# Performance work log

Measured on AMD Instinct MI355X. Metric: run time of the kernel, lower is better.

Reference implementation:

```python
import jax, jax.numpy as jnp
import numpy as np

H = 32        # query heads
KVH = 8       # key/value heads
D = 64        # head_dim
HID = 2048
B, S = 2, 2048

def rotate_half(x):
    x1, x2 = x[..., :D // 2], x[..., D // 2:]
    return jnp.concatenate((-x2, x1), axis=-1)

def setup_inputs() -> dict:
    key = jax.random.key(0)
    ks = jax.random.split(key, 7)
    scale = 1.0 / np.sqrt(HID)
    return {
        "x": jax.random.normal(ks[0], (B, S, HID), jnp.float32),
        "cos": jax.random.uniform(ks[1], (S, D), jnp.float32),
        "sin": jax.random.uniform(ks[2], (S, D), jnp.float32),
        "wq": jax.random.normal(ks[3], (HID, H * D), jnp.float32) * scale,
        "wk": jax.random.normal(ks[4], (HID, KVH * D), jnp.float32) * scale,
        "wv": jax.random.normal(ks[5], (HID, KVH * D), jnp.float32) * scale,
        "wo": jax.random.normal(ks[6], (HID, HID), jnp.float32) * scale,
    }

def reference(x, cos, sin, wq, wk, wv, wo):
    b, s, _ = x.shape
    # QKV projections -> [b, heads, s, d]
    q = (x @ wq).reshape(b, s, H, D).transpose(0, 2, 1, 3)
    k = (x @ wk).reshape(b, s, KVH, D).transpose(0, 2, 1, 3)
    v = (x @ wv).reshape(b, s, KVH, D).transpose(0, 2, 1, 3)
    # RoPE (cos/sin broadcast over batch and heads)
    c = cos[None, None, :, :]
    si = sin[None, None, :, :]
    q = q * c + rotate_half(q) * si
    k = k * c + rotate_half(k) * si
    # GQA: expand kv heads (repeat_interleave on head axis)
    g = H // KVH
    k = jnp.repeat(k, g, axis=1)
    v = jnp.repeat(v, g, axis=1)
    # causal SDPA
    scores = jnp.einsum("bhqd,bhkd->bhqk", q, k) / np.sqrt(D).astype(np.float32)
    causal = jnp.tril(jnp.ones((s, s), dtype=bool))
    scores = jnp.where(causal[None, None], scores, jnp.finfo(scores.dtype).min)
    attn = jax.nn.softmax(scores, axis=-1)
    out = jnp.einsum("bhqk,bhkd->bhqd", attn, v)
    out = out.transpose(0, 2, 1, 3).reshape(b, s, H * D)
    return out @ wo
```

## Files before the change

### kernel.cpp

```cpp
#include <hip/hip_runtime.h>
#include <stdint.h>

#define B_ 2
#define S_ 2048
#define H_ 32
#define KVH_ 8
#define D_ 64
#define HID_ 2048

typedef float f32x4 __attribute__((ext_vector_type(4)));
typedef float f32x16 __attribute__((ext_vector_type(16)));
typedef short bf16x8 __attribute__((ext_vector_type(8)));
typedef unsigned short u16;
typedef unsigned short u16x4 __attribute__((ext_vector_type(4)));
typedef unsigned short u16x8 __attribute__((ext_vector_type(8)));
typedef unsigned int u32;
typedef unsigned int u32x2 __attribute__((ext_vector_type(2)));
typedef unsigned int u32x4 __attribute__((ext_vector_type(4)));

__device__ __forceinline__ u16 f2b(float f) {
  unsigned u = __builtin_bit_cast(unsigned, f);
  u += 0x7fffu + ((u >> 16) & 1u);
  return (u16)(u >> 16);
}
__device__ __forceinline__ float b2f(u16 h) {
  unsigned u = ((unsigned)h) << 16;
  return __builtin_bit_cast(float, u);
}
__device__ __forceinline__ void gl_lds16(const void* g, void* l) {
  __builtin_amdgcn_global_load_lds(
      (const __attribute__((address_space(1))) unsigned*)g,
      (__attribute__((address_space(3))) unsigned*)l, 16, 0, 0);
}
__device__ __forceinline__ f32x4 mfma16(bf16x8 a, bf16x8 b, f32x4 c) {
  return __builtin_amdgcn_mfma_f32_16x16x32_bf16(a, b, c, 0, 0, 0);
}
__device__ __forceinline__ f32x16 mfma32(bf16x8 a, bf16x8 b, f32x16 c) {
  return __builtin_amdgcn_mfma_f32_32x32x16_bf16(a, b, c, 0, 0, 0);
}
__device__ __forceinline__ u32 cvtpk(float lo, float hi) {
  u32 r;
  asm("v_cvt_pk_bf16_f32 %0, %1, %2" : "=v"(r) : "v"(lo), "v"(hi));
  return r;
}
__device__ __forceinline__ float fast_exp2(float x) {
#if __has_builtin(__builtin_amdgcn_exp2f)
  return __builtin_amdgcn_exp2f(x);
#else
  return exp2f(x);
#endif
}
__device__ __forceinline__ void swap32(u32 a, u32 b, u32& x, u32& y) {
#if __has_builtin(__builtin_amdgcn_permlane32_swap)
  auto r = __builtin_amdgcn_permlane32_swap(a, b, false, false);
  x = r[0];
  y = r[1];
#else
  u32 sa = (u32)__shfl_xor((int)a, 32), sb = (u32)__shfl_xor((int)b, 32);
  bool hib = (threadIdx.x & 32) != 0;
  x = hib ? sb : a;
  y = hib ? b : sa;
#endif
}

__global__ __launch_bounds__(256) void k_cvt(const float* __restrict__ src,
                                             u16* __restrict__ dst, int n4) {
  int i = blockIdx.x * 256 + threadIdx.x;
  if (i >= n4) return;
  f32x4 v = *(const f32x4*)(src + (size_t)i * 4);
  u16x4 o;
  o[0] = f2b(v[0]); o[1] = f2b(v[1]); o[2] = f2b(v[2]); o[3] = f2b(v[3]);
  *(u16x4*)(dst + (size_t)i * 4) = o;
}

__global__ __launch_bounds__(256) void k_transpose(const float* __restrict__ src,
                                                   u16* __restrict__ dst,
                                                   int K, int N) {
  __shared__ float t[32][33];
  int n0 = blockIdx.x * 32, k0 = blockIdx.y * 32;
  int tt = threadIdx.x;
  int r = tt >> 3, c4 = (tt & 7) << 2;
  f32x4 v = *(const f32x4*)(src + (size_t)(k0 + r) * N + n0 + c4);
  t[r][c4 + 0] = v[0]; t[r][c4 + 1] = v[1];
  t[r][c4 + 2] = v[2]; t[r][c4 + 3] = v[3];
  __syncthreads();
  u16x4 o;
  o[0] = f2b(t[c4 + 0][r]); o[1] = f2b(t[c4 + 1][r]);
  o[2] = f2b(t[c4 + 2][r]); o[3] = f2b(t[c4 + 3][r]);
  *(u16x4*)(dst + (size_t)(n0 + r) * K + k0 + c4) = o;
}

__device__ __forceinline__ void stage64(const u16* __restrict__ G, int rowbase,
                                        int K, int kt, u16* unit, int tid) {
  int r = tid >> 3, sl = tid & 7;
  gl_lds16(G + (size_t)(rowbase + r) * K + kt * 64 + ((sl ^ (r & 7)) << 3),
           (char*)unit + tid * 16);
}

template <int BN, int OUTF32>
__global__ __launch_bounds__(512, 1) void k_gemm8(const u16* __restrict__ A,
                                                  const u16* __restrict__ BT,
                                                  float* __restrict__ Cf,
                                                  u16* __restrict__ Cb,
                                                  int M, int N, int K) {
  constexpr int ATILE = 256 * 64;
  constexpr int BTILE = BN * 64;
  constexpr int BU = BN / 64;
  constexpr int WN = (BN == 128) ? 2 : 4;
  constexpr int NI = (BN == 192) ? 3 : 4;
  constexpr int MI = (BN == 128) ? 4 : 8;
  constexpr int MIP = MI / 4;
  __shared__ __align__(16) u16 sm[2 * ATILE + 2 * BTILE];
  const int tid = threadIdx.x;
  const int l = tid & 63;
  const int lg = (l >> 4) & 3, lr = l & 15;
  const int w = tid >> 6;
  const int wm = w / WN, wn = w % WN;

  const int nwg = gridDim.x;
  const int cpx = nwg >> 3;
  const int bid = blockIdx.x;
  const int swz = (bid & 7) * cpx + (bid >> 3);
  const int ntn = N / BN;
  const int bm = swz / ntn, bn = swz % ntn;
  const int m0 = bm << 8, n0 = bn * BN;

  const u16* Ag = A + (size_t)m0 * K;
  const u16* Bg = BT + (size_t)n0 * K;
  u16* As = sm;
  u16* Bs = sm + 2 * ATILE;

  const int nt = K >> 6;
  f32x4 acc[MI][NI] = {};

#pragma unroll
  for (int u = 0; u < 4; ++u) stage64(Ag, u * 64, K, 0, As + u * 4096, tid);
#pragma unroll
  for (int u = 0; u < BU; ++u) stage64(Bg, u * 64, K, 0, Bs + u * 4096, tid);
  stage64(Ag, 0, K, 1, As + ATILE, tid);
  stage64(Ag, 64, K, 1, As + ATILE + 4096, tid);
  asm volatile("s_waitcnt vmcnt(2)" ::: "memory");
  __builtin_amdgcn_s_barrier();
  asm volatile("" ::: "memory");

  for (int t = 0; t < nt; ++t) {
    const int cur = t & 1;
    u16* Ac = As + cur * ATILE;
    u16* Bc = Bs + cur * BTILE;
    u16* An = As + (cur ^ 1) * ATILE;
    u16* Bn = Bs + (cur ^ 1) * BTILE;
    bf16x8 bc[NI][2];
#pragma unroll
    for (int q = 0; q < 4; ++q) {
      bf16x8 af[MIP][2];
#pragma unroll
      for (int mi2 = 0; mi2 < MIP; ++mi2)
#pragma unroll
        for (int ks = 0; ks < 2; ++ks) {
          int row = wm * (MI * 16) + (q * MIP + mi2) * 16 + lr;
          int slot = (ks * 4 + lg) ^ (lr & 7);
          af[mi2][ks] = *(const bf16x8*)&Ac[row * 64 + slot * 8];
        }
      if (q == 0) {
#pragma unroll
        for (int ni = 0; ni < NI; ++ni)
#pragma unroll
          for (int ks = 0; ks < 2; ++ks) {
            int row = wn * (NI * 16) + ni * 16 + lr;
            int slot = (ks * 4 + lg) ^ (lr & 7);
            bc[ni][ks] = *(const bf16x8*)&Bc[row * 64 + slot * 8];
          }
      }
      if (t + 1 < nt) {
        if (q == 0) {
          stage64(Ag, 128, K, t + 1, An + 2 * 4096, tid);
          stage64(Ag, 192, K, t + 1, An + 3 * 4096, tid);
        } else if (q == 1) {
          stage64(Bg, 0, K, t + 1, Bn, tid);
          stage64(Bg, 64, K, t + 1, Bn + 4096, tid);
        } else if (q == 2) {
          if (BU >= 3) stage64(Bg, 128, K, t + 1, Bn + 2 * 4096, tid);
          if (BU >= 4) stage64(Bg, 192, K, t + 1, Bn + 3 * 4096, tid);
        }
      }
      __builtin_amdgcn_s_barrier();
      asm volatile("" ::: "memory");
      __builtin_amdgcn_s_setprio(1);
#pragma unroll
      for (int mi2 = 0; mi2 < MIP; ++mi2)
#pragma unroll
        for (int ni = 0; ni < NI; ++ni)
#pragma unroll
          for (int ks = 0; ks < 2; ++ks)
            acc[q * MIP + mi2][ni] =
                mfma16(af[mi2][ks], bc[ni][ks], acc[q * MIP + mi2][ni]);
      __builtin_amdgcn_s_setprio(0);
      if (q == 3) {
        if (t + 2 < nt) {
          stage64(Ag, 0, K, t + 2, Ac, tid);
          stage64(Ag, 64, K, t + 2, Ac + 4096, tid);
          asm volatile("s_waitcnt vmcnt(2)" ::: "memory");
        } else if (t + 1 < nt) {
          asm volatile("s_waitcnt vmcnt(0)" ::: "memory");
        }
      }
      __builtin_amdgcn_s_barrier();
      asm volatile("" ::: "memory");
    }
  }

#pragma unroll
  for (int mi = 0; mi < MI; ++mi)
#pragma unroll
    for (int ni = 0; ni < NI; ++ni)
#pragma unroll
      for (int j = 0; j < 4; ++j) {
        size_t row = (size_t)m0 + wm * (MI * 16) + mi * 16 + lg * 4 + j;
        size_t col = (size_t)n0 + wn * (NI * 16) + ni * 16 + lr;
        if (OUTF32)
          Cf[row * N + col] = acc[mi][ni][j];
        else
          Cb[row * N + col] = f2b(acc[mi][ni][j]);
      }
}

__global__ __launch_bounds__(256) void k_rope(const u16* __restrict__ qkv,
                                              const float* __restrict__ cosb,
                                              const float* __restrict__ sinb,
                                              u16* __restrict__ Qr,
                                              u16* __restrict__ Kr) {
  int task = blockIdx.x * 4 + (threadIdx.x >> 6);
  int l = threadIdx.x & 63;
  int head = task % (H_ + KVH_);
  int row = task / (H_ + KVH_);
  int b = row >> 11, s = row & (S_ - 1);
  float c = cosb[s * 64 + l], si = sinb[s * 64 + l];
  const u16* base = qkv + (size_t)row * 3072;
  float val;
  if (head < H_)
    val = b2f(base[head * 64 + l]);
  else
    val = b2f(base[2048 + (head - H_) * 64 + l]);
  float partner = __shfl_xor(val, 32);
  float rot = (l < 32) ? -partner : partner;
  float out = val * c + rot * si;
  if (head < H_)
    Qr[((size_t)(b * H_ + head) * S_ + s) * 64 + l] = f2b(out * 0.18033688f);
  else
    Kr[((size_t)(b * KVH_ + (head - H_)) * S_ + s) * 64 + l] = f2b(out);
}

__global__ __launch_bounds__(256) void k_vtrans(const u16* __restrict__ qkv,
                                                u16* __restrict__ Vt) {
  int bid = blockIdx.x;
  int st = bid & 31, kvh = (bid >> 5) & 7, b = bid >> 8;
  int s0 = st * 64;
  __shared__ u16 t[64][72];
  int tid = threadIdx.x;
  int sl = tid >> 2, c16 = (tid & 3) << 4;
  const u16* src = qkv + (size_t)(b * S_ + s0 + sl) * 3072 + 2560 + kvh * 64 + c16;
  u16x8 v0 = *(const u16x8*)src;
  u16x8 v1 = *(const u16x8*)(src + 8);
#pragma unroll
  for (int i = 0; i < 8; ++i) { t[sl][c16 + i] = v0[i]; t[sl][c16 + 8 + i] = v1[i]; }
  __syncthreads();
  int dl = tid >> 2, s16 = (tid & 3) << 4;
  u16x8 o0, o1;
#pragma unroll
  for (int i = 0; i < 8; ++i) { o0[i] = t[s16 + i][dl]; o1[i] = t[s16 + 8 + i][dl]; }
  u16* dst = Vt + ((size_t)(b * KVH_ + kvh) * 64 + dl) * S_ + s0 + s16;
  *(u16x8*)dst = o0;
  *(u16x8*)(dst + 8) = o1;
}

__device__ __forceinline__ void stage_kv(const u16* __restrict__ Kg,
                                         const u16* __restrict__ Vg, int k0,
                                         u16* ldsK, u16* ldsV, int tid) {
#pragma unroll
  for (int p = 0; p < 2; ++p) {
    int id2 = p * 256 + tid;
    int r = id2 >> 3, cc = id2 & 7;
    gl_lds16(Kg + (size_t)(k0 + r) * 64 + ((cc ^ (r & 7)) << 3), ldsK + id2 * 8);
  }
#pragma unroll
  for (int p = 0; p < 2; ++p) {
    int id2 = p * 256 + tid;
    int dd = id2 >> 3, cc = id2 & 7;
    gl_lds16(Vg + (size_t)dd * S_ + k0 + ((cc ^ (dd & 7)) << 3), ldsV + id2 * 8);
  }
}

__device__ __forceinline__ void repack2(const f32x16 s, bf16x8& f0, bf16x8& f1) {
  bf16x8 outv[2];
#pragma unroll
  for (int h = 0; h < 2; ++h) {
    u32 a0 = cvtpk(s[8 * h + 0], s[8 * h + 1]);
    u32 a1 = cvtpk(s[8 * h + 4], s[8 * h + 5]);
    u32 b0 = cvtpk(s[8 * h + 2], s[8 * h + 3]);
    u32 b1 = cvtpk(s[8 * h + 6], s[8 * h + 7]);
    u32 x0, y0, x1, y1;
    swap32(a0, a1, x0, y0);
    swap32(b0, b1, x1, y1);
    u32x4 t;
    t[0] = x0; t[1] = x1; t[2] = y0; t[3] = y1;
    outv[h] = __builtin_bit_cast(bf16x8, t);
  }
  f0 = outv[0];
  f1 = outv[1];
}

__global__ __launch_bounds__(256) void k_attn(const u16* __restrict__ Q,
                                              const u16* __restrict__ Kr,
                                              const u16* __restrict__ Vt,
                                              u16* __restrict__ Oout) {
  __shared__ __align__(16) u16 lds[16384];
  const int tid = threadIdx.x;
  const int w = tid >> 6, l = tid & 63;
  const int hi = l >> 5, l31 = l & 31;

  const int bid = blockIdx.x;
  const int b = bid & 1;
  const int hh = (bid >> 1) & 31;
  const int pp = bid >> 6;
  const int kvh = hh >> 2;

  int off8[4];
#pragma unroll
  for (int c = 0; c < 4; ++c)
    off8[c] = l31 * 64 + ((((c << 1) | hi) ^ (l31 & 7)) << 3);

  const u16* Kg = Kr + (size_t)(b * KVH_ + kvh) * S_ * 64;
  const u16* Vg = Vt + (size_t)(b * KVH_ + kvh) * 64 * S_;

  for (int seg = 0; seg < 2; ++seg) {
    const int qtl = (seg == 0) ? pp : 15 - pp;
    const int q0 = qtl * 128;
    const int qw0 = q0 + w * 32;
    const int nt = 2 * qtl + 2;

    const size_t qrow = (size_t)((b * H_ + hh) * S_ + qw0 + l31) * 64;
    bf16x8 qf[4];
#pragma unroll
    for (int c = 0; c < 4; ++c)
      qf[c] = *(const bf16x8*)&Q[qrow + c * 16 + hi * 8];

    f32x16 o0 = {}, o1 = {};
    float l_run = 0.f;

    stage_kv(Kg, Vg, 0, lds, lds + 8192, tid);
    asm volatile("s_waitcnt vmcnt(0)" ::: "memory");
    __builtin_amdgcn_s_barrier();
    asm volatile("" ::: "memory");

    for (int kt = 0; kt < nt; ++kt) {
      const int cur = kt & 1;
      const int k0 = kt * 64;
      if (kt + 1 < nt)
        stage_kv(Kg, Vg, k0 + 64, lds + (cur ^ 1) * 4096,
                 lds + 8192 + (cur ^ 1) * 4096, tid);

      if (k0 <= qw0 + 31) {
        const u16* Kc = lds + cur * 4096;
        const u16* Vc = lds + 8192 + cur * 4096;

        f32x16 sl = {}, sh = {};
        __builtin_amdgcn_s_setprio(1);
#pragma unroll
        for (int c = 0; c < 4; ++c) {
          bf16x8 klo = *(const bf16x8*)(Kc + off8[c]);
          bf16x8 khi = *(const bf16x8*)(Kc + 2048 + off8[c]);
          sl = mfma32(klo, qf[c], sl);
          sh = mfma32(khi, qf[c], sh);
        }
        __builtin_amdgcn_s_setprio(0);

        if (k0 + 63 > qw0) {
          int qg = qw0 + l31;
#pragma unroll
          for (int r = 0; r < 16; ++r) {
            int kg = k0 + (r & 3) + 8 * (r >> 2) + 4 * hi;
            if (kg > qg) sl[r] = -3e38f;
            if (kg + 32 > qg) sh[r] = -3e38f;
          }
        }

        float smv[16];
#pragma unroll
        for (int i = 0; i < 16; ++i) {
          sl[i] = fast_exp2(sl[i]);
          sh[i] = fast_exp2(sh[i]);
          smv[i] = sl[i] + sh[i];
        }
#pragma unroll
        for (int i = 0; i < 8; ++i) smv[i] += smv[i + 8];
#pragma unroll
        for (int i = 0; i < 4; ++i) smv[i] += smv[i + 4];
        smv[0] = (smv[0] + smv[2]) + (smv[1] + smv[3]);
        l_run += smv[0] + __shfl_xor(smv[0], 32);

        bf16x8 pf[4];
        repack2(sl, pf[0], pf[1]);
        repack2(sh, pf[2], pf[3]);

        __builtin_amdgcn_s_setprio(1);
#pragma unroll
        for (int sub = 0; sub < 4; ++sub) {
          bf16x8 v0 = *(const bf16x8*)(Vc + off8[sub]);
          bf16x8 v1 = *(const bf16x8*)(Vc + 2048 + off8[sub]);
          o0 = mfma32(v0, pf[sub], o0);
          o1 = mfma32(v1, pf[sub], o1);
        }
        __builtin_amdgcn_s_setprio(0);
      }

      asm volatile("s_waitcnt vmcnt(0)" ::: "memory");
      __builtin_amdgcn_s_barrier();
      asm volatile("" ::: "memory");
    }

    {
      u16* ep = lds + w * 2304;
      float inv = 1.0f / l_run;
      float oc[32];
#pragma unroll
      for (int i = 0; i < 16; ++i) { oc[i] = o0[i]; oc[16 + i] = o1[i]; }
#pragma unroll
      for (int dh = 0; dh < 2; ++dh)
#pragma unroll
        for (int g = 0; g < 4; ++g) {
          u32 w0 = cvtpk(oc[dh * 16 + 4 * g + 0] * inv, oc[dh * 16 + 4 * g + 1] * inv);
          u32 w1 = cvtpk(oc[dh * 16 + 4 * g + 2] * inv, oc[dh * 16 + 4 * g + 3] * inv);
          int col = dh * 32 + 8 * g + 4 * hi;
          u32x2 tw; tw[0] = w0; tw[1] = w1;
          *(u32x2*)&ep[l31 * 72 + col] = tw;
        }
      asm volatile("s_waitcnt lgkmcnt(0)" ::: "memory");
      int row = l >> 1;
      size_t gb = ((size_t)(b * S_ + q0 + w * 32 + row)) * HID_ + hh * 64 + (l & 1) * 32;
#pragma unroll
      for (int cc = 0; cc < 4; ++cc) {
        u16x8 v = *(const u16x8*)&ep[row * 72 + (l & 1) * 32 + cc * 8];
        *(u16x8*)&Oout[gb + cc * 8] = v;
      }
    }
    __syncthreads();
  }
}

extern "C" void kernel_launch(void* const* d_in, const int* in_sizes, int n_in,
                              void* d_out, int out_size, void* d_ws, size_t ws_size,
                              hipStream_t stream) {
  (void)in_sizes; (void)n_in; (void)out_size; (void)ws_size;
  const float* x    = (const float*)d_in[0];
  const float* cosb = (const float*)d_in[1];
  const float* sinb = (const float*)d_in[2];
  const float* wq   = (const float*)d_in[3];
  const float* wk   = (const float*)d_in[4];
  const float* wv   = (const float*)d_in[5];
  const float* wo   = (const float*)d_in[6];

  char* wsb = (char*)d_ws;
  u16* xb    = (u16*)(wsb + 0);
  u16* wqkvT = (u16*)(wsb + 16777216);
  u16* woT   = (u16*)(wsb + 29360128);
  u16* qkv   = (u16*)(wsb + 37748736);
  u16* attno = qkv;
  u16* Qr    = (u16*)(wsb + 62914560);
  u16* Kr    = (u16*)(wsb + 79691776);
  u16* Vt    = (u16*)(wsb + 83886080);

  k_cvt<<<8192, 256, 0, stream>>>(x, xb, (B_ * S_ * HID_) / 4);
  k_transpose<<<dim3(64, 64), 256, 0, stream>>>(wq, wqkvT, 2048, 2048);
  k_transpose<<<dim3(16, 64), 256, 0, stream>>>(wk, wqkvT + (size_t)2048 * 2048, 2048, 512);
  k_transpose<<<dim3(16, 64), 256, 0, stream>>>(wv, wqkvT + (size_t)2560 * 2048, 2048, 512);
  k_transpose<<<dim3(64, 64), 256, 0, stream>>>(wo, woT, 2048, 2048);

  k_gemm8<192, 0><<<256, 512, 0, stream>>>(xb, wqkvT, nullptr, qkv, 4096, 3072, 2048);

  k_rope<<<40960, 256, 0, stream>>>(qkv, cosb, sinb, Qr, Kr);
  k_vtrans<<<512, 256, 0, stream>>>(qkv, Vt);

  k_attn<<<512, 256, 0, stream>>>(Qr, Kr, Vt, attno);

  k_gemm8<128, 1><<<256, 512, 0, stream>>>(attno, woT, (float*)d_out, nullptr,
                                           4096, 2048, 2048);
}
```

Before: 196.8 us.

## Use 8-wave attention blocks over 256-query tiles and vectorize RoPE

The attention kernel now runs 512 threads per block, each block covering a 256-row query tile. This replaces the earlier 128-row tiles that were processed in paired segments for causal load balance. Blocks are launched heaviest tile first, and each thread stages one K and one V chunk per 64-key tile. The RoPE kernel now handles 16 lanes per head row with two-element vector loads and stores instead of one element per lane plus a shuffle. The changes aim to share each K/V tile across more query rows and to cut RoPE launch and instruction overhead, at the cost of relying on heavy-first ordering instead of explicit pairing for load balance.

```diff
diff --git a/kernel.cpp b/kernel.cpp
--- a/kernel.cpp
+++ b/kernel.cpp
@@ -229,25 +229,32 @@
                                               const float* __restrict__ sinb,
                                               u16* __restrict__ Qr,
                                               u16* __restrict__ Kr) {
-  int task = blockIdx.x * 4 + (threadIdx.x >> 6);
-  int l = threadIdx.x & 63;
+  int task = blockIdx.x * 16 + (threadIdx.x >> 4);
+  int t16 = threadIdx.x & 15;
   int head = task % (H_ + KVH_);
   int row = task / (H_ + KVH_);
   int b = row >> 11, s = row & (S_ - 1);
-  float c = cosb[s * 64 + l], si = sinb[s * 64 + l];
-  const u16* base = qkv + (size_t)row * 3072;
-  float val;
-  if (head < H_)
-    val = b2f(base[head * 64 + l]);
-  else
-    val = b2f(base[2048 + (head - H_) * 64 + l]);
-  float partner = __shfl_xor(val, 32);
-  float rot = (l < 32) ? -partner : partner;
-  float out = val * c + rot * si;
-  if (head < H_)
-    Qr[((size_t)(b * H_ + head) * S_ + s) * 64 + l] = f2b(out * 0.18033688f);
-  else
-    Kr[((size_t)(b * KVH_ + (head - H_)) * S_ + s) * 64 + l] = f2b(out);
+  int d2 = t16 * 2;
+  const u16* base =
+      qkv + (size_t)row * 3072 + (head < H_ ? head * 64 : 2048 + (head - H_) * 64);
+  u32 lo = *(const u32*)(base + d2);
+  u32 hi = *(const u32*)(base + d2 + 32);
+  float xl0 = b2f((u16)lo), xl1 = b2f((u16)(lo >> 16));
+  float xh0 = b2f((u16)hi), xh1 = b2f((u16)(hi >> 16));
+  const float* cb = cosb + s * 64;
+  const float* sb = sinb + s * 64;
+  float cl0 = cb[d2], cl1 = cb[d2 + 1], ch0 = cb[d2 + 32], ch1 = cb[d2 + 33];
+  float sl0 = sb[d2], sl1 = sb[d2 + 1], sh0 = sb[d2 + 32], sh1 = sb[d2 + 33];
+  float sc = (head < H_) ? 0.18033688f : 1.0f;
+  float ol0 = (xl0 * cl0 - xh0 * sl0) * sc;
+  float ol1 = (xl1 * cl1 - xh1 * sl1) * sc;
+  float oh0 = (xh0 * ch0 + xl0 * sh0) * sc;
+  float oh1 = (xh1 * ch1 + xl1 * sh1) * sc;
+  u16* dst = (head < H_)
+                 ? Qr + ((size_t)(b * H_ + head) * S_ + s) * 64
+                 : Kr + ((size_t)(b * KVH_ + (head - H_)) * S_ + s) * 64;
+  *(u32*)(dst + d2) = (u32)f2b(ol0) | ((u32)f2b(ol1) << 16);
+  *(u32*)(dst + d2 + 32) = (u32)f2b(oh0) | ((u32)f2b(oh1) << 16);
 }
 
 __global__ __launch_bounds__(256) void k_vtrans(const u16* __restrict__ qkv,
@@ -273,21 +280,12 @@
   *(u16x8*)(dst + 8) = o1;
 }
 
-__device__ __forceinline__ void stage_kv(const u16* __restrict__ Kg,
-                                         const u16* __restrict__ Vg, int k0,
-                                         u16* ldsK, u16* ldsV, int tid) {
-#pragma unroll
-  for (int p = 0; p < 2; ++p) {
-    int id2 = p * 256 + tid;
-    int r = id2 >> 3, cc = id2 & 7;
-    gl_lds16(Kg + (size_t)(k0 + r) * 64 + ((cc ^ (r & 7)) << 3), ldsK + id2 * 8);
-  }
-#pragma unroll
-  for (int p = 0; p < 2; ++p) {
-    int id2 = p * 256 + tid;
-    int dd = id2 >> 3, cc = id2 & 7;
-    gl_lds16(Vg + (size_t)dd * S_ + k0 + ((cc ^ (dd & 7)) << 3), ldsV + id2 * 8);
-  }
+__device__ __forceinline__ void stage_kv8(const u16* __restrict__ Kg,
+                                          const u16* __restrict__ Vg, int k0,
+                                          u16* ldsK, u16* ldsV, int tid) {
+  int r = tid >> 3, cc = tid & 7;
+  gl_lds16(Kg + (size_t)(k0 + r) * 64 + ((cc ^ (r & 7)) << 3), ldsK + tid * 8);
+  gl_lds16(Vg + (size_t)r * S_ + k0 + ((cc ^ (r & 7)) << 3), ldsV + tid * 8);
 }
 
 __device__ __forceinline__ void repack2(const f32x16 s, bf16x8& f0, bf16x8& f1) {
@@ -309,7 +307,7 @@
   f1 = outv[1];
 }
 
-__global__ __launch_bounds__(256) void k_attn(const u16* __restrict__ Q,
+__global__ __launch_bounds__(512) void k_attn(const u16* __restrict__ Q,
                                               const u16* __restrict__ Kr,
                                               const u16* __restrict__ Vt,
                                               u16* __restrict__ Oout) {
@@ -319,131 +317,126 @@
   const int hi = l >> 5, l31 = l & 31;
 
   const int bid = blockIdx.x;
+  const int qtl = 7 - (bid >> 6);
+  const int hh = (bid >> 1) & 31;
   const int b = bid & 1;
-  const int hh = (bid >> 1) & 31;
-  const int pp = bid >> 6;
   const int kvh = hh >> 2;
+  const int q0 = qtl * 256;
+  const int qw0 = q0 + w * 32;
+  const int nt = 4 * qtl + 4;
 
   int off8[4];
 #pragma unroll
   for (int c = 0; c < 4; ++c)
     off8[c] = l31 * 64 + ((((c << 1) | hi) ^ (l31 & 7)) << 3);
 
+  const size_t qrow = (size_t)((b * H_ + hh) * S_ + qw0 + l31) * 64;
+  bf16x8 qf[4];
+#pragma unroll
+  for (int c = 0; c < 4; ++c)
+    qf[c] = *(const bf16x8*)&Q[qrow + c * 16 + hi * 8];
+
   const u16* Kg = Kr + (size_t)(b * KVH_ + kvh) * S_ * 64;
   const u16* Vg = Vt + (size_t)(b * KVH_ + kvh) * 64 * S_;
 
-  for (int seg = 0; seg < 2; ++seg) {
-    const int qtl = (seg == 0) ? pp : 15 - pp;
-    const int q0 = qtl * 128;
-    const int qw0 = q0 + w * 32;
-    const int nt = 2 * qtl + 2;
-
-    const size_t qrow = (size_t)((b * H_ + hh) * S_ + qw0 + l31) * 64;
-    bf16x8 qf[4];
-#pragma unroll
-    for (int c = 0; c < 4; ++c)
-      qf[c] = *(const bf16x8*)&Q[qrow + c * 16 + hi * 8];
-
-    f32x16 o0 = {}, o1 = {};
-    float l_run = 0.f;
-
-    stage_kv(Kg, Vg, 0, lds, lds + 8192, tid);
+  f32x16 o0 = {}, o1 = {};
+  float l_run = 0.f;
+
+  stage_kv8(Kg, Vg, 0, lds, lds + 4096, tid);
+  asm volatile("s_waitcnt vmcnt(0)" ::: "memory");
+  __builtin_amdgcn_s_barrier();
+  asm volatile("" ::: "memory");
+
+  for (int kt = 0; kt < nt; ++kt) {
+    const int cur = kt & 1;
+    const int k0 = kt * 64;
+    if (kt + 1 < nt)
+      stage_kv8(Kg, Vg, k0 + 64, lds + (cur ^ 1) * 8192,
+                lds + (cur ^ 1) * 8192 + 4096, tid);
+
+    if (k0 <= qw0 + 31) {
+      const u16* Kc = lds + cur * 8192;
+      const u16* Vc = Kc + 4096;
+
+      f32x16 sl = {}, sh = {};
+      __builtin_amdgcn_s_setprio(1);
+#pragma unroll
+      for (int c = 0; c < 4; ++c) {
+        bf16x8 klo = *(const bf16x8*)(Kc + off8[c]);
+        bf16x8 khi = *(const bf16x8*)(Kc + 2048 + off8[c]);
+        sl = mfma32(klo, qf[c], sl);
+        sh = mfma32(khi, qf[c], sh);
+      }
+      __builtin_amdgcn_s_setprio(0);
+
+      if (k0 + 63 > qw0) {
+        int qg = qw0 + l31;
+#pragma unroll
+        for (int r = 0; r < 16; ++r) {
+          int kg = k0 + (r & 3) + 8 * (r >> 2) + 4 * hi;
+          if (kg > qg) sl[r] = -3e38f;
+          if (kg + 32 > qg) sh[r] = -3e38f;
+        }
+      }
+
+      float smv[16];
+#pragma unroll
+      for (int i = 0; i < 16; ++i) {
+        sl[i] = fast_exp2(sl[i]);
+        sh[i] = fast_exp2(sh[i]);
+        smv[i] = sl[i] + sh[i];
+      }
+#pragma unroll
+      for (int i = 0; i < 8; ++i) smv[i] += smv[i + 8];
+#pragma unroll
+      for (int i = 0; i < 4; ++i) smv[i] += smv[i + 4];
+      smv[0] = (smv[0] + smv[2]) + (smv[1] + smv[3]);
+      l_run += smv[0] + __shfl_xor(smv[0], 32);
+
+      bf16x8 pf[4];
+      repack2(sl, pf[0], pf[1]);
+      repack2(sh, pf[2], pf[3]);
+
+      __builtin_amdgcn_s_setprio(1);
+#pragma unroll
+      for (int sub = 0; sub < 4; ++sub) {
+        bf16x8 v0 = *(const bf16x8*)(Vc + off8[sub]);
+        bf16x8 v1 = *(const bf16x8*)(Vc + 2048 + off8[sub]);
+        o0 = mfma32(v0, pf[sub], o0);
+        o1 = mfma32(v1, pf[sub], o1);
+      }
+      __builtin_amdgcn_s_setprio(0);
+    }
+
     asm volatile("s_waitcnt vmcnt(0)" ::: "memory");
     __builtin_amdgcn_s_barrier();
     asm volatile("" ::: "memory");
-
-    for (int kt = 0; kt < nt; ++kt) {
-      const int cur = kt & 1;
-      const int k0 = kt * 64;
-      if (kt + 1 < nt)
-        stage_kv(Kg, Vg, k0 + 64, lds + (cur ^ 1) * 4096,
-                 lds + 8192 + (cur ^ 1) * 4096, tid);
-
-      if (k0 <= qw0 + 31) {
-        const u16* Kc = lds + cur * 4096;
-        const u16* Vc = lds + 8192 + cur * 4096;
-
-        f32x16 sl = {}, sh = {};
-        __builtin_amdgcn_s_setprio(1);
-#pragma unroll
-        for (int c = 0; c < 4; ++c) {
-          bf16x8 klo = *(const bf16x8*)(Kc + off8[c]);
-          bf16x8 khi = *(const bf16x8*)(Kc + 2048 + off8[c]);
-          sl = mfma32(klo, qf[c], sl);
-          sh = mfma32(khi, qf[c], sh);
-        }
-        __builtin_amdgcn_s_setprio(0);
-
-        if (k0 + 63 > qw0) {
-          int qg = qw0 + l31;
-#pragma unroll
-          for (int r = 0; r < 16; ++r) {
-            int kg = k0 + (r & 3) + 8 * (r >> 2) + 4 * hi;
-            if (kg > qg) sl[r] = -3e38f;
-            if (kg + 32 > qg) sh[r] = -3e38f;
-          }
-        }
-
-        float smv[16];
-#pragma unroll
-        for (int i = 0; i < 16; ++i) {
-          sl[i] = fast_exp2(sl[i]);
-          sh[i] = fast_exp2(sh[i]);
-          smv[i] = sl[i] + sh[i];
-        }
-#pragma unroll
-        for (int i = 0; i < 8; ++i) smv[i] += smv[i + 8];
-#pragma unroll
-        for (int i = 0; i < 4; ++i) smv[i] += smv[i + 4];
-        smv[0] = (smv[0] + smv[2]) + (smv[1] + smv[3]);
-        l_run += smv[0] + __shfl_xor(smv[0], 32);
-
-        bf16x8 pf[4];
-        repack2(sl, pf[0], pf[1]);
-        repack2(sh, pf[2], pf[3]);
-
-        __builtin_amdgcn_s_setprio(1);
-#pragma unroll
-        for (int sub = 0; sub < 4; ++sub) {
-          bf16x8 v0 = *(const bf16x8*)(Vc + off8[sub]);
-          bf16x8 v1 = *(const bf16x8*)(Vc + 2048 + off8[sub]);
-          o0 = mfma32(v0, pf[sub], o0);
-          o1 = mfma32(v1, pf[sub], o1);
-        }
-        __builtin_amdgcn_s_setprio(0);
-      }
-
-      asm volatile("s_waitcnt vmcnt(0)" ::: "memory");
-      __builtin_amdgcn_s_barrier();
-      asm volatile("" ::: "memory");
+  }
+
+  {
+    u16* ep = lds + w * 2048;
+    float inv = 1.0f / l_run;
+    float oc[32];
+#pragma unroll
+    for (int i = 0; i < 16; ++i) { oc[i] = o0[i]; oc[16 + i] = o1[i]; }
+#pragma unroll
+    for (int dh = 0; dh < 2; ++dh)
+#pragma unroll
+      for (int g = 0; g < 4; ++g) {
+        u32 w0 = cvtpk(oc[dh * 16 + 4 * g + 0] * inv, oc[dh * 16 + 4 * g + 1] * inv);
+        u32 w1 = cvtpk(oc[dh * 16 + 4 * g + 2] * inv, oc[dh * 16 + 4 * g + 3] * inv);
+        int col = dh * 32 + 8 * g + 4 * hi;
+        u32x2 tw; tw[0] = w0; tw[1] = w1;
+        *(u32x2*)&ep[l31 * 64 + col] = tw;
+      }
+    asm volatile("s_waitcnt lgkmcnt(0)" ::: "memory");
+    int row = l >> 1;
+    size_t gb = ((size_t)(b * S_ + q0 + w * 32 + row)) * HID_ + hh * 64 + (l & 1) * 32;
+#pragma unroll
+    for (int cc = 0; cc < 4; ++cc) {
+      u16x8 v = *(const u16x8*)&ep[row * 64 + (l & 1) * 32 + cc * 8];
+      *(u16x8*)&Oout[gb + cc * 8] = v;
     }
-
-    {
-      u16* ep = lds + w * 2304;
-      float inv = 1.0f / l_run;
-      float oc[32];
-#pragma unroll
-      for (int i = 0; i < 16; ++i) { oc[i] = o0[i]; oc[16 + i] = o1[i]; }
-#pragma unroll
-      for (int dh = 0; dh < 2; ++dh)
-#pragma unroll
-        for (int g = 0; g < 4; ++g) {
-          u32 w0 = cvtpk(oc[dh * 16 + 4 * g + 0] * inv, oc[dh * 16 + 4 * g + 1] * inv);
-          u32 w1 = cvtpk(oc[dh * 16 + 4 * g + 2] * inv, oc[dh * 16 + 4 * g + 3] * inv);
-          int col = dh * 32 + 8 * g + 4 * hi;
-          u32x2 tw; tw[0] = w0; tw[1] = w1;
-          *(u32x2*)&ep[l31 * 72 + col] = tw;
-        }
-      asm volatile("s_waitcnt lgkmcnt(0)" ::: "memory");
-      int row = l >> 1;
-      size_t gb = ((size_t)(b * S_ + q0 + w * 32 + row)) * HID_ + hh * 64 + (l & 1) * 32;
-#pragma unroll
-      for (int cc = 0; cc < 4; ++cc) {
-        u16x8 v = *(const u16x8*)&ep[row * 72 + (l & 1) * 32 + cc * 8];
-        *(u16x8*)&Oout[gb + cc * 8] = v;
-      }
-    }
-    __syncthreads();
   }
 }
 
@@ -477,10 +470,10 @@
 
   k_gemm8<192, 0><<<256, 512, 0, stream>>>(xb, wqkvT, nullptr, qkv, 4096, 3072, 2048);
 
-  k_rope<<<40960, 256, 0, stream>>>(qkv, cosb, sinb, Qr, Kr);
+  k_rope<<<10240, 256, 0, stream>>>(qkv, cosb, sinb, Qr, Kr);
   k_vtrans<<<512, 256, 0, stream>>>(qkv, Vt);
 
-  k_attn<<<512, 256, 0, stream>>>(Qr, Kr, Vt, attno);
+  k_attn<<<512, 512, 0, stream>>>(Qr, Kr, Vt, attno);
 
   k_gemm8<128, 1><<<256, 512, 0, stream>>>(attno, woT, (float*)d_out, nullptr,
                                            4096, 2048, 2048);
```

Measured after the change: 185.1 us. 6.0% less time.
